# Kernel tuning notes

Measured on AMD Instinct MI355X. Metric: run time of the kernel, lower is better.

The kernel has to match this reference:

```python
import jax, jax.numpy as jnp
import numpy as np

D = 256; NH = 8; NL = 4; NP = 4; DFF = 1024; BS = 8; NQ = 300
DH = D // NH
EPS = 1e-5
SPATIAL = np.array([[100, 150], [50, 75], [25, 38], [13, 19]], dtype=np.int64)  # (H, W) per level
SIZES = (SPATIAL[:, 0] * SPATIAL[:, 1])
S = int(SIZES.sum())  # 19947
LSI = np.concatenate([[0], np.cumsum(SIZES)[:-1]]).astype(np.int64)


def setup_inputs() -> dict:
    key = jax.random.key(0)
    ks = iter(jax.random.split(key, 48))
    def nrm(shape, s=0.02):
        return jax.random.normal(next(ks), shape, jnp.float32) * s
    return {
        "tgt": jax.random.normal(next(ks), (BS, NQ, D), jnp.float32),
        "tgt_query_pos": jax.random.normal(next(ks), (BS, NQ, D), jnp.float32),
        "tgt_reference_points": jax.random.uniform(next(ks), (BS, NQ, NL, 2), jnp.float32),
        "memory": jax.random.normal(next(ks), (BS, S, D), jnp.float32),
        "memory_key_padding_mask": jnp.zeros((BS, S), jnp.bool_),
        "memory_spatial_shapes": jnp.asarray(SPATIAL),
        "memory_level_start_index": jnp.asarray(LSI),
        # self-attention (nn.MultiheadAttention) params
        "in_proj_w": nrm((3 * D, D)), "in_proj_b": jnp.zeros((3 * D,), jnp.float32),
        "out_proj_w": nrm((D, D)), "out_proj_b": jnp.zeros((D,), jnp.float32),
        # layernorms
        "norm1_g": jnp.ones((D,), jnp.float32), "norm1_b": jnp.zeros((D,), jnp.float32),
        "norm2_g": jnp.ones((D,), jnp.float32), "norm2_b": jnp.zeros((D,), jnp.float32),
        "norm3_g": jnp.ones((D,), jnp.float32), "norm3_b": jnp.zeros((D,), jnp.float32),
        # MSDeformAttn params
        "samp_off_w": nrm((NH * NL * NP * 2, D)), "samp_off_b": nrm((NH * NL * NP * 2,), 0.5),
        "attn_wt_w": nrm((NH * NL * NP, D)), "attn_wt_b": jnp.zeros((NH * NL * NP,), jnp.float32),
        "value_w": nrm((D, D)), "value_b": jnp.zeros((D,), jnp.float32),
        "outp_w": nrm((D, D)), "outp_b": jnp.zeros((D,), jnp.float32),
        # FFN params
        "lin1_w": nrm((DFF, D)), "lin1_b": jnp.zeros((DFF,), jnp.float32),
        "lin2_w": nrm((D, DFF)), "lin2_b": jnp.zeros((D,), jnp.float32),
    }


def _ln(x, g, b):
    m = x.mean(-1, keepdims=True)
    v = ((x - m) ** 2).mean(-1, keepdims=True)
    return (x - m) / jnp.sqrt(v + EPS) * g + b


def _self_attn(tgt, pos, in_w, in_b, ow, ob):
    bs, nq, _ = tgt.shape
    qk = tgt + pos
    qw, kw, vw = jnp.split(in_w, 3, axis=0)
    qb, kb, vb = jnp.split(in_b, 3)
    proj = lambda x, w, b: (x @ w.T + b).reshape(bs, nq, NH, DH)
    qh, kh, vh = proj(qk, qw, qb), proj(qk, kw, kb), proj(tgt, vw, vb)
    logits = jnp.einsum('bqhd,bkhd->bhqk', qh, kh) / np.sqrt(DH).astype(np.float32)
    a = jax.nn.softmax(logits, axis=-1)
    o = jnp.einsum('bhqk,bkhd->bqhd', a, vh).reshape(bs, nq, D)
    return o @ ow.T + ob


def _msdeform(query, ref, memory, pad_mask, so_w, so_b, aw_w, aw_b, vw, vb, ow, ob):
    bs, nq, _ = query.shape
    value = memory @ vw.T + vb
    value = jnp.where(pad_mask[..., None], 0.0, value).reshape(bs, S, NH, DH)
    off = (query @ so_w.T + so_b).reshape(bs, nq, NH, NL, NP, 2)
    aw = jax.nn.softmax((query @ aw_w.T + aw_b).reshape(bs, nq, NH, NL * NP), axis=-1)
    aw = aw.reshape(bs, nq, NH, NL, NP)
    # offset normalizer is (W, H) per level
    normalizer = jnp.asarray(SPATIAL[:, ::-1].copy(), jnp.float32)
    locs = ref[:, :, None, :, None, :] + off / normalizer[None, None, None, :, None, :]
    out = jnp.zeros((bs, nq, NH, DH), jnp.float32)
    for l in range(NL):
        Hl, Wl = int(SPATIAL[l, 0]), int(SPATIAL[l, 1])
        s0 = int(LSI[l])
        v = value[:, s0:s0 + Hl * Wl]  # [bs, Hl*Wl, NH, DH]
        # grid_sample(align_corners=False) pixel mapping
        x = locs[:, :, :, l, :, 0] * Wl - 0.5  # [bs, nq, NH, NP]
        y = locs[:, :, :, l, :, 1] * Hl - 0.5
        x0f, y0f = jnp.floor(x), jnp.floor(y)
        tx, ty = x - x0f, y - y0f
        x0, y0 = x0f.astype(jnp.int32), y0f.astype(jnp.int32)
        samp = jnp.zeros(x.shape + (DH,), jnp.float32)
        for dy, dx, w in ((0, 0, (1 - ty) * (1 - tx)), (0, 1, (1 - ty) * tx),
                          (1, 0, ty * (1 - tx)), (1, 1, ty * tx)):
            xi, yi = x0 + dx, y0 + dy
            valid = (xi >= 0) & (xi < Wl) & (yi >= 0) & (yi < Hl)  # zero padding
            idx = jnp.clip(yi, 0, Hl - 1) * Wl + jnp.clip(xi, 0, Wl - 1)
            idx2 = idx.swapaxes(2, 3).reshape(bs, nq * NP, NH)
            g = jnp.take_along_axis(v, idx2[..., None], axis=1)  # [bs, nq*NP, NH, DH]
            g = g.reshape(bs, nq, NP, NH, DH).transpose(0, 1, 3, 2, 4)
            samp = samp + g * (w * valid)[..., None]
        out = out + jnp.einsum('bqhp,bqhpd->bqhd', aw[:, :, :, l], samp)
    return out.reshape(bs, nq, D) @ ow.T + ob


def reference(tgt, tgt_query_pos, tgt_reference_points, memory, memory_key_padding_mask,
              memory_spatial_shapes, memory_level_start_index,
              in_proj_w, in_proj_b, out_proj_w, out_proj_b,
              norm1_g, norm1_b, norm2_g, norm2_b, norm3_g, norm3_b,
              samp_off_w, samp_off_b, attn_wt_w, attn_wt_b,
              value_w, value_b, outp_w, outp_b,
              lin1_w, lin1_b, lin2_w, lin2_b):
    # self-cross ordering (self_cross=True), eval mode (dropout=identity)
    t2 = _self_attn(tgt, tgt_query_pos, in_proj_w, in_proj_b, out_proj_w, out_proj_b)
    tgt = _ln(tgt + t2, norm2_g, norm2_b)
    t2 = _msdeform(tgt + tgt_query_pos, tgt_reference_points, memory, memory_key_padding_mask,
                   samp_off_w, samp_off_b, attn_wt_w, attn_wt_b, value_w, value_b, outp_w, outp_b)
    tgt = _ln(tgt + t2, norm1_g, norm1_b)
    t2 = jax.nn.relu(tgt @ lin1_w.T + lin1_b) @ lin2_w.T + lin2_b
    return _ln(tgt + t2, norm3_g, norm3_b)
```

## Files before the change

kernel.cpp:

```cpp
#include <hip/hip_runtime.h>
#include <hip/hip_bf16.h>

#define D_   256
#define NH_  8
#define NL_  4
#define NP_  4
#define DFF_ 1024
#define BS_  8
#define NQ_  300
#define DH_  32
#define S_TOT 19947
#define EPS_ 1e-5f

typedef __bf16 bf16x8 __attribute__((ext_vector_type(8)));
typedef __bf16 bf16x4 __attribute__((ext_vector_type(4)));
typedef float  f32x4  __attribute__((ext_vector_type(4)));

#define W_INW  0
#define W_OUTW 196608
#define W_SOW  262144
#define W_AWW  327680
#define W_VW   360448
#define W_OPW  425984
#define W_L1W  491520
#define W_L2W  753664
#define W_TOT  1015808

__global__ __launch_bounds__(256) void cast_w_kernel(
    const float* __restrict__ s_inw, const float* __restrict__ s_outw,
    const float* __restrict__ s_sow, const float* __restrict__ s_aww,
    const float* __restrict__ s_vw,  const float* __restrict__ s_opw,
    const float* __restrict__ s_l1w, const float* __restrict__ s_l2w,
    __bf16* __restrict__ dst)
{
    const int i = (blockIdx.x * 256 + threadIdx.x) * 4;
    if (i >= W_TOT) return;
    const float* s; int off;
    if      (i < W_OUTW) { s = s_inw;  off = W_INW;  }
    else if (i < W_SOW)  { s = s_outw; off = W_OUTW; }
    else if (i < W_AWW)  { s = s_sow;  off = W_SOW;  }
    else if (i < W_VW)   { s = s_aww;  off = W_AWW;  }
    else if (i < W_OPW)  { s = s_vw;   off = W_VW;   }
    else if (i < W_L1W)  { s = s_opw;  off = W_OPW;  }
    else if (i < W_L2W)  { s = s_l1w;  off = W_L1W;  }
    else                 { s = s_l2w;  off = W_L2W;  }
    const float4 v = *(const float4*)(s + (i - off));
    bf16x4 o;
    o[0] = (__bf16)v.x; o[1] = (__bf16)v.y;
    o[2] = (__bf16)v.z; o[3] = (__bf16)v.w;
    *(bf16x4*)(dst + i) = o;
}

__global__ __launch_bounds__(256) void rearrange_vw_kernel(
    const __bf16* __restrict__ W, __bf16* __restrict__ Wf)
{
    const int g = blockIdx.x * 256 + threadIdx.x;
    const int l = g & 63;
    const int t = (g >> 6) & 15;
    const int s = g >> 10;
    const int row = t * 16 + (l & 15);
    const int col = s * 32 + (l >> 4) * 8;
    *(bf16x8*)(Wf + (size_t)g * 8) = *(const bf16x8*)(W + (size_t)row * 256 + col);
}

__global__ __launch_bounds__(512, 4) void gemm_value(
    const float* __restrict__ A, const __bf16* __restrict__ Wf,
    const float* __restrict__ bias, __hip_bfloat16* __restrict__ C, int M)
{
    __shared__ __align__(16) __bf16 As[2][16][264];
    const int tid = threadIdx.x;
    const int wave = tid >> 6, lane = tid & 63;
    const int frow = lane & 15;
    const int k8 = (lane >> 4) * 8;

    bf16x8 bB[2][8];
#pragma unroll
    for (int j = 0; j < 2; ++j) {
        const int t = wave * 2 + j;
#pragma unroll
        for (int s = 0; s < 8; ++s)
            bB[j][s] = *(const bf16x8*)(Wf + ((size_t)(s * 16 + t) * 64 + lane) * 8);
    }
    float bb0 = bias[wave * 32 + frow];
    float bb1 = bias[wave * 32 + 16 + frow];

    const int nt = (M + 15) >> 4;
    const int stride = gridDim.x;
    int tile = blockIdx.x;

    const int srow = tid >> 5;
    const int scol = (tid & 31) * 8;

    {
        int gr = tile * 16 + srow; if (gr >= M) gr = M - 1;
        const float* ap = A + (size_t)gr * 256 + scol;
        const float4 a0 = *(const float4*)ap;
        const float4 a1 = *(const float4*)(ap + 4);
        bf16x8 o;
        o[0] = (__bf16)a0.x; o[1] = (__bf16)a0.y;
        o[2] = (__bf16)a0.z; o[3] = (__bf16)a0.w;
        o[4] = (__bf16)a1.x; o[5] = (__bf16)a1.y;
        o[6] = (__bf16)a1.z; o[7] = (__bf16)a1.w;
        *(bf16x8*)&As[0][srow][scol] = o;
    }
    __syncthreads();

    int buf = 0;
    for (; tile < nt; tile += stride, buf ^= 1) {
        const int nxt = tile + stride;
        const bool have_nxt = nxt < nt;
        float4 p0, p1;
        if (have_nxt) {
            int gr = nxt * 16 + srow; if (gr >= M) gr = M - 1;
            const float* ap = A + (size_t)gr * 256 + scol;
            p0 = *(const float4*)ap;
            p1 = *(const float4*)(ap + 4);
        }

        f32x4 acc0 = (f32x4){0.f, 0.f, 0.f, 0.f};
        f32x4 acc1 = acc0;
#pragma unroll
        for (int s = 0; s < 8; ++s) {
            const bf16x8 aF = *(const bf16x8*)&As[buf][frow][s * 32 + k8];
            acc0 = __builtin_amdgcn_mfma_f32_16x16x32_bf16(aF, bB[0][s], acc0, 0, 0, 0);
            acc1 = __builtin_amdgcn_mfma_f32_16x16x32_bf16(aF, bB[1][s], acc1, 0, 0, 0);
        }

        const int m0 = tile * 16;
        const int row0 = (lane >> 4) * 4;
        const int col0 = wave * 32 + frow;
#pragma unroll
        for (int r = 0; r < 4; ++r) {
            const int gr = m0 + row0 + r;
            if (gr < M) {
                __hip_bfloat16* cp = C + (size_t)gr * 256 + col0;
                cp[0]  = __float2bfloat16(acc0[r] + bb0);
                cp[16] = __float2bfloat16(acc1[r] + bb1);
            }
        }

        if (have_nxt) {
            bf16x8 o;
            o[0] = (__bf16)p0.x; o[1] = (__bf16)p0.y;
            o[2] = (__bf16)p0.z; o[3] = (__bf16)p0.w;
            o[4] = (__bf16)p1.x; o[5] = (__bf16)p1.y;
            o[6] = (__bf16)p1.z; o[7] = (__bf16)p1.w;
            *(bf16x8*)&As[buf ^ 1][srow][scol] = o;
        }
        __syncthreads();
    }
}

__global__ __launch_bounds__(256) void gemm_small(
    const float* __restrict__ A, const float* __restrict__ A2,
    const __bf16* __restrict__ W, const float* __restrict__ bias,
    float* __restrict__ C, int M, int N, int K, int relu)
{
    __shared__ __align__(16) __bf16 As[64][40];
    __shared__ __align__(16) __bf16 Bs[64][40];
    const int tid = threadIdx.x;
    const int wave = tid >> 6, lane = tid & 63;
    const int m0 = blockIdx.x * 64, n0 = blockIdx.y * 64;
    const int frow = lane & 15, fk = (lane >> 4) * 8;

    f32x4 acc[4];
#pragma unroll
    for (int j = 0; j < 4; ++j) acc[j] = (f32x4){0.f, 0.f, 0.f, 0.f};

    const int ar = tid >> 2;
    const int ak = (tid & 3) * 8;
    const bool a_ok = (m0 + ar) < M;

    for (int k0 = 0; k0 < K; k0 += 32) {
        float4 a0 = make_float4(0,0,0,0), a1 = a0;
        if (a_ok) {
            const float* ap = A + (size_t)(m0 + ar) * K + k0 + ak;
            a0 = *(const float4*)ap;
            a1 = *(const float4*)(ap + 4);
            if (A2) {
                const float* ap2 = A2 + (size_t)(m0 + ar) * K + k0 + ak;
                const float4 c0 = *(const float4*)ap2;
                const float4 c1 = *(const float4*)(ap2 + 4);
                a0.x += c0.x; a0.y += c0.y; a0.z += c0.z; a0.w += c0.w;
                a1.x += c1.x; a1.y += c1.y; a1.z += c1.z; a1.w += c1.w;
            }
        }
        const bf16x8 b8 = *(const bf16x8*)(W + (size_t)(n0 + ar) * K + k0 + ak);

        __syncthreads();
        bf16x8 w0;
        w0[0] = (__bf16)a0.x; w0[1] = (__bf16)a0.y; w0[2] = (__bf16)a0.z; w0[3] = (__bf16)a0.w;
        w0[4] = (__bf16)a1.x; w0[5] = (__bf16)a1.y; w0[6] = (__bf16)a1.z; w0[7] = (__bf16)a1.w;
        *(bf16x8*)&As[ar][ak] = w0;
        *(bf16x8*)&Bs[ar][ak] = b8;
        __syncthreads();

        const bf16x8 aF = *(const bf16x8*)&As[wave * 16 + frow][fk];
#pragma unroll
        for (int j = 0; j < 4; ++j) {
            const bf16x8 bF = *(const bf16x8*)&Bs[j * 16 + frow][fk];
            acc[j] = __builtin_amdgcn_mfma_f32_16x16x32_bf16(aF, bF, acc[j], 0, 0, 0);
        }
    }

    const int row = m0 + wave * 16 + (lane >> 4) * 4;
#pragma unroll
    for (int j = 0; j < 4; ++j) {
        const int col = n0 + j * 16 + frow;
        const float bb = bias[col];
#pragma unroll
        for (int r = 0; r < 4; ++r) {
            if (row + r >= M) continue;
            float val = acc[j][r] + bb;
            if (relu) val = fmaxf(val, 0.f);
            C[(size_t)(row + r) * N + col] = val;
        }
    }
}

__global__ __launch_bounds__(256) void attn_logits_kernel(
    const float* __restrict__ qk, __bf16* __restrict__ P)
{
    const int qt = blockIdx.x, bh = blockIdx.y;
    const int b = bh >> 3, h = bh & 7;
    const int wave = threadIdx.x >> 6, lane = threadIdx.x & 63;
    const int m = qt * 64 + wave * 16 + (lane & 15);
    const int k8 = (lane >> 4) * 8;
    const float scale = 0.17677669529663687f;

    bf16x8 aF = {};
    if (m < NQ_) {
        const float* qp = qk + (size_t)(b * NQ_ + m) * 512 + h * 32 + k8;
        const float4 q0 = *(const float4*)qp;
        const float4 q1 = *(const float4*)(qp + 4);
        aF[0] = (__bf16)q0.x; aF[1] = (__bf16)q0.y;
        aF[2] = (__bf16)q0.z; aF[3] = (__bf16)q0.w;
        aF[4] = (__bf16)q1.x; aF[5] = (__bf16)q1.y;
        aF[6] = (__bf16)q1.z; aF[7] = (__bf16)q1.w;
    }

    f32x4 c[19];
#pragma unroll
    for (int t = 0; t < 19; ++t) {
        const int n = t * 16 + (lane & 15);
        bf16x8 bF = {};
        if (n < NQ_) {
            const float* kp = qk + (size_t)(b * NQ_ + n) * 512 + 256 + h * 32 + k8;
            const float4 k0 = *(const float4*)kp;
            const float4 k1 = *(const float4*)(kp + 4);
            bF[0] = (__bf16)k0.x; bF[1] = (__bf16)k0.y;
            bF[2] = (__bf16)k0.z; bF[3] = (__bf16)k0.w;
            bF[4] = (__bf16)k1.x; bF[5] = (__bf16)k1.y;
            bF[6] = (__bf16)k1.z; bF[7] = (__bf16)k1.w;
        }
        f32x4 z = (f32x4){0.f, 0.f, 0.f, 0.f};
        c[t] = __builtin_amdgcn_mfma_f32_16x16x32_bf16(aF, bF, z, 0, 0, 0);
    }

    const int myc = lane & 15;
#pragma unroll
    for (int t = 0; t < 19; ++t) {
        const bool ok = (t * 16 + myc) < NQ_;
#pragma unroll
        for (int r = 0; r < 4; ++r)
            c[t][r] = ok ? c[t][r] * scale : -1e30f;
    }

    float mx[4] = {-1e30f, -1e30f, -1e30f, -1e30f};
#pragma unroll
    for (int t = 0; t < 19; ++t)
#pragma unroll
        for (int r = 0; r < 4; ++r) mx[r] = fmaxf(mx[r], c[t][r]);
#pragma unroll
    for (int off = 8; off; off >>= 1)
#pragma unroll
        for (int r = 0; r < 4; ++r)
            mx[r] = fmaxf(mx[r], __shfl_xor(mx[r], off, 64));

    float sum[4] = {0.f, 0.f, 0.f, 0.f};
#pragma unroll
    for (int t = 0; t < 19; ++t)
#pragma unroll
        for (int r = 0; r < 4; ++r) {
            const float e = __expf(c[t][r] - mx[r]);
            c[t][r] = e;
            sum[r] += e;
        }
#pragma unroll
    for (int off = 8; off; off >>= 1)
#pragma unroll
        for (int r = 0; r < 4; ++r)
            sum[r] += __shfl_xor(sum[r], off, 64);
    float inv[4];
#pragma unroll
    for (int r = 0; r < 4; ++r) inv[r] = 1.f / sum[r];

    __bf16* Pr = P + (size_t)bh * NQ_ * 320;
    const int row0 = qt * 64 + wave * 16 + (lane >> 4) * 4;
#pragma unroll
    for (int t = 0; t < 19; ++t) {
        const int col = t * 16 + myc;
        if (col >= NQ_) continue;
#pragma unroll
        for (int r = 0; r < 4; ++r)
            if (row0 + r < NQ_)
                Pr[(size_t)(row0 + r) * 320 + col] = (__bf16)(c[t][r] * inv[r]);
    }
}

__global__ __launch_bounds__(256) void attn_pv_kernel(
    const __bf16* __restrict__ P, const float* __restrict__ v,
    float* __restrict__ attn)
{
    __shared__ __align__(16) __bf16 Vt[32][328];
    const int qt = blockIdx.x, bh = blockIdx.y;
    const int b = bh >> 3, h = bh & 7;
    const int tid = threadIdx.x;

    {
        const int d = tid & 31;
        for (int kk = tid >> 5; kk < NQ_; kk += 8)
            Vt[d][kk] = (__bf16)v[(size_t)(b * NQ_ + kk) * 256 + h * 32 + d];
        for (int i = tid; i < 32 * 20; i += 256)
            Vt[i & 31][300 + (i >> 5)] = (__bf16)0.f;
    }
    __syncthreads();

    const int wave = tid >> 6, lane = tid & 63;
    const int mrow = qt * 64 + wave * 16 + (lane & 15);
    const int k8 = (lane >> 4) * 8;
    const __bf16* Pr = P + (size_t)bh * NQ_ * 320;

    f32x4 acc0 = (f32x4){0.f, 0.f, 0.f, 0.f};
    f32x4 acc1 = acc0;
#pragma unroll
    for (int k0 = 0; k0 < 320; k0 += 32) {
        bf16x8 aF = {};
        if (mrow < NQ_) aF = *(const bf16x8*)(Pr + (size_t)mrow * 320 + k0 + k8);
        const bf16x8 b0 = *(const bf16x8*)&Vt[lane & 15][k0 + k8];
        const bf16x8 b1 = *(const bf16x8*)&Vt[16 + (lane & 15)][k0 + k8];
        acc0 = __builtin_amdgcn_mfma_f32_16x16x32_bf16(aF, b0, acc0, 0, 0, 0);
        acc1 = __builtin_amdgcn_mfma_f32_16x16x32_bf16(aF, b1, acc1, 0, 0, 0);
    }

    const int row0 = qt * 64 + wave * 16 + (lane >> 4) * 4;
    const int col = lane & 15;
#pragma unroll
    for (int r = 0; r < 4; ++r) {
        if (row0 + r >= NQ_) continue;
        float* op = attn + (size_t)(b * NQ_ + row0 + r) * 256 + h * 32;
        op[col]      = acc0[r];
        op[col + 16] = acc1[r];
    }
}

__global__ __launch_bounds__(256) void ln_kernel(
    const float* __restrict__ x, const float* __restrict__ res,
    const float* __restrict__ g, const float* __restrict__ bt,
    float* __restrict__ out,
    const float* __restrict__ pos, float* __restrict__ out2)
{
    const int row = blockIdx.x;
    const int tid = threadIdx.x;
    const size_t idx = (size_t)row * D_ + tid;
    float v = x[idx] + (res ? res[idx] : 0.f);

    __shared__ float red[4];
    float s = v;
#pragma unroll
    for (int off = 32; off; off >>= 1) s += __shfl_xor(s, off, 64);
    if ((tid & 63) == 0) red[tid >> 6] = s;
    __syncthreads();
    const float mean = (red[0] + red[1] + red[2] + red[3]) * (1.f / D_);
    const float c = v - mean;
    __syncthreads();

    float s2 = c * c;
#pragma unroll
    for (int off = 32; off; off >>= 1) s2 += __shfl_xor(s2, off, 64);
    if ((tid & 63) == 0) red[tid >> 6] = s2;
    __syncthreads();
    const float var = (red[0] + red[1] + red[2] + red[3]) * (1.f / D_);

    const float y = c * rsqrtf(var + EPS_) * g[tid] + bt[tid];
    out[idx] = y;
    if (out2) out2[idx] = y + pos[idx];
}

__global__ __launch_bounds__(256) void msdeform_kernel(
    const float* __restrict__ offs, const float* __restrict__ awl,
    const float* __restrict__ refp, const __hip_bfloat16* __restrict__ value,
    float* __restrict__ samp)
{
    const int row = blockIdx.x;
    const int b = row / NQ_;
    const int tid = threadIdx.x;
    const int h = tid >> 5, d = tid & 31;

    __shared__ float off_s[256];
    __shared__ float aw_s[128];
    __shared__ float ref_s[8];
    off_s[tid] = offs[(size_t)row * 256 + tid];
    if (tid < 128) aw_s[tid] = awl[(size_t)row * 128 + tid];
    if (tid < 8) ref_s[tid] = refp[(size_t)row * 8 + tid];
    __syncthreads();

    float mx = -1e30f;
#pragma unroll
    for (int i = 0; i < 16; ++i) mx = fmaxf(mx, aw_s[h * 16 + i]);
    float sum = 0.f;
#pragma unroll
    for (int i = 0; i < 16; ++i) sum += __expf(aw_s[h * 16 + i] - mx);
    const float winv = 1.f / sum;

    const int Hs[4] = {100, 50, 25, 13};
    const int Wl_[4] = {150, 75, 38, 19};
    const int S0[4] = {0, 15000, 18750, 19700};

    float o = 0.f;
    const __hip_bfloat16* vbase = value + ((size_t)b * S_TOT) * D_ + h * 32 + d;

#pragma unroll
    for (int l = 0; l < NL_; ++l) {
        const int Hl = Hs[l], Wl = Wl_[l];
        const float rx = ref_s[l * 2], ry = ref_s[l * 2 + 1];
        const __hip_bfloat16* vl = vbase + (size_t)S0[l] * D_;
#pragma unroll
        for (int p = 0; p < NP_; ++p) {
            const int oi = ((h * NL_ + l) * NP_ + p) * 2;
            const float lx = rx + off_s[oi] / (float)Wl;
            const float ly = ry + off_s[oi + 1] / (float)Hl;
            const float x = lx * Wl - 0.5f;
            const float y = ly * Hl - 0.5f;
            const float x0f = floorf(x), y0f = floorf(y);
            const float tx = x - x0f, ty = y - y0f;
            const int x0 = (int)x0f, y0 = (int)y0f;
            const float aw = __expf(aw_s[h * 16 + l * 4 + p] - mx) * winv;

            float sacc = 0.f;
#pragma unroll
            for (int cc = 0; cc < 4; ++cc) {
                const int dy = cc >> 1, dx = cc & 1;
                const int xi = x0 + dx, yi = y0 + dy;
                const float w = (dy ? ty : 1.f - ty) * (dx ? tx : 1.f - tx);
                if (xi >= 0 && xi < Wl && yi >= 0 && yi < Hl) {
                    const int idx = yi * Wl + xi;
                    sacc += w * __bfloat162float(vl[(size_t)idx * D_]);
                }
            }
            o += aw * sacc;
        }
    }
    samp[(size_t)row * 256 + tid] = o;
}

extern "C" void kernel_launch(void* const* d_in, const int* in_sizes, int n_in,
                              void* d_out, int out_size, void* d_ws, size_t ws_size,
                              hipStream_t stream)
{
    const float* tgt   = (const float*)d_in[0];
    const float* pos   = (const float*)d_in[1];
    const float* refp  = (const float*)d_in[2];
    const float* memory= (const float*)d_in[3];
    const float* in_w  = (const float*)d_in[7];
    const float* in_b  = (const float*)d_in[8];
    const float* outw  = (const float*)d_in[9];
    const float* outb  = (const float*)d_in[10];
    const float* n1g = (const float*)d_in[11]; const float* n1b = (const float*)d_in[12];
    const float* n2g = (const float*)d_in[13]; const float* n2b = (const float*)d_in[14];
    const float* n3g = (const float*)d_in[15]; const float* n3b = (const float*)d_in[16];
    const float* sow = (const float*)d_in[17]; const float* sob = (const float*)d_in[18];
    const float* aww = (const float*)d_in[19]; const float* awb = (const float*)d_in[20];
    const float* vw  = (const float*)d_in[21]; const float* vb_ = (const float*)d_in[22];
    const float* opw = (const float*)d_in[23]; const float* opb = (const float*)d_in[24];
    const float* l1w = (const float*)d_in[25]; const float* l1b = (const float*)d_in[26];
    const float* l2w = (const float*)d_in[27]; const float* l2b = (const float*)d_in[28];
    float* out = (float*)d_out;

    char* ws = (char*)d_ws;
    size_t o = 0;
    auto alloc = [&](size_t bytes) -> char* {
        char* p = ws + o;
        o += (bytes + 255) & ~(size_t)255;
        return p;
    };

    const int M = BS_ * NQ_;
    __bf16* Wb = (__bf16*)alloc((size_t)W_TOT * 2);
    __bf16* Wf = (__bf16*)alloc((size_t)65536 * 2);
    __hip_bfloat16* value = (__hip_bfloat16*)alloc((size_t)BS_ * S_TOT * D_ * 2);
    __bf16* P    = (__bf16*)alloc((size_t)64 * NQ_ * 320 * 2);
    float* qk    = (float*)alloc((size_t)M * 512 * 4);
    float* v     = (float*)alloc((size_t)M * 256 * 4);
    float* attn  = (float*)alloc((size_t)M * 256 * 4);
    float* attno = (float*)alloc((size_t)M * 256 * 4);
    float* tgt1  = (float*)alloc((size_t)M * 256 * 4);
    float* query2= (float*)alloc((size_t)M * 256 * 4);
    float* offs  = (float*)alloc((size_t)M * 256 * 4);
    float* awl   = (float*)alloc((size_t)M * 128 * 4);
    float* samp  = (float*)alloc((size_t)M * 256 * 4);
    float* t2m   = (float*)alloc((size_t)M * 256 * 4);
    float* tgt2  = (float*)alloc((size_t)M * 256 * 4);
    float* ffn1  = (float*)alloc((size_t)M * 1024 * 4);
    float* ffn2  = (float*)alloc((size_t)M * 256 * 4);

    const dim3 blk(256);
    const int MB = (M + 63) / 64;

    cast_w_kernel<<<(W_TOT / 4 + 255) / 256, blk, 0, stream>>>(
        in_w, outw, sow, aww, vw, opw, l1w, l2w, Wb);
    rearrange_vw_kernel<<<32, blk, 0, stream>>>(Wb + W_VW, Wf);

    gemm_small<<<dim3(MB, 8), blk, 0, stream>>>(tgt, pos, Wb + W_INW, in_b, qk, M, 512, 256, 0);
    gemm_small<<<dim3(MB, 4), blk, 0, stream>>>(tgt, nullptr, Wb + W_INW + 512 * 256, in_b + 512, v, M, 256, 256, 0);
    attn_logits_kernel<<<dim3(5, 64), blk, 0, stream>>>(qk, P);
    attn_pv_kernel<<<dim3(5, 64), blk, 0, stream>>>(P, v, attn);
    gemm_small<<<dim3(MB, 4), blk, 0, stream>>>(attn, nullptr, Wb + W_OUTW, outb, attno, M, 256, 256, 0);
    ln_kernel<<<M, blk, 0, stream>>>(tgt, attno, n2g, n2b, tgt1, pos, query2);

    gemm_small<<<dim3(MB, 4), blk, 0, stream>>>(query2, nullptr, Wb + W_SOW, sob, offs, M, 256, 256, 0);
    gemm_small<<<dim3(MB, 2), blk, 0, stream>>>(query2, nullptr, Wb + W_AWW, awb, awl, M, 128, 256, 0);
    gemm_value<<<dim3(512), dim3(512), 0, stream>>>(memory, Wf, vb_, value, BS_ * S_TOT);
    msdeform_kernel<<<M, blk, 0, stream>>>(offs, awl, refp, value, samp);
    gemm_small<<<dim3(MB, 4), blk, 0, stream>>>(samp, nullptr, Wb + W_OPW, opb, t2m, M, 256, 256, 0);
    ln_kernel<<<M, blk, 0, stream>>>(tgt1, t2m, n1g, n1b, tgt2, nullptr, nullptr);

    gemm_small<<<dim3(MB, 16), blk, 0, stream>>>(tgt2, nullptr, Wb + W_L1W, l1b, ffn1, M, 1024, 256, 1);
    gemm_small<<<dim3(MB, 4), blk, 0, stream>>>(ffn1, nullptr, Wb + W_L2W, l2b, ffn2, M, 256, 1024, 0);
    ln_kernel<<<M, blk, 0, stream>>>(tgt2, ffn2, n3g, n3b, out, nullptr, nullptr);
}
```

Measured before the change: 476.8 us.

## Fuse self-attention logits and PV, merge offset/weight GEMMs, vectorize deform sampling

The softmax-logits and P·V kernels are merged into one kernel that keeps the probability tile in shared memory instead of writing it to global memory. The sampling-offset and attention-weight projections become a single GEMM launch that writes to two outputs. The deformable-sampling kernel now handles two queries per block, and each thread reads two bf16 channels with one 32-bit load. Together these cut launches, global round-trips and per-channel gather loads, at the cost of more shared memory per block in the fused attention kernel.

```diff
diff --git a/kernel.cpp b/kernel.cpp
--- a/kernel.cpp
+++ b/kernel.cpp
@@ -154,7 +154,8 @@
 __global__ __launch_bounds__(256) void gemm_small(
     const float* __restrict__ A, const float* __restrict__ A2,
     const __bf16* __restrict__ W, const float* __restrict__ bias,
-    float* __restrict__ C, int M, int N, int K, int relu)
+    float* __restrict__ C, int M, int N, int K, int relu,
+    const float* __restrict__ bias2, float* __restrict__ C2, int N1)
 {
     __shared__ __align__(16) __bf16 As[64][40];
     __shared__ __align__(16) __bf16 Bs[64][40];
@@ -207,26 +208,44 @@
 #pragma unroll
     for (int j = 0; j < 4; ++j) {
         const int col = n0 + j * 16 + frow;
-        const float bb = bias[col];
+        float* dst; const float* bsrc; int strideC, ccol;
+        if (!C2 || col < N1) { dst = C;  bsrc = bias;  strideC = N1;     ccol = col; }
+        else                 { dst = C2; bsrc = bias2; strideC = N - N1; ccol = col - N1; }
+        const float bb = bsrc[ccol];
 #pragma unroll
         for (int r = 0; r < 4; ++r) {
             if (row + r >= M) continue;
             float val = acc[j][r] + bb;
             if (relu) val = fmaxf(val, 0.f);
-            C[(size_t)(row + r) * N + col] = val;
-        }
-    }
-}
-
-__global__ __launch_bounds__(256) void attn_logits_kernel(
-    const float* __restrict__ qk, __bf16* __restrict__ P)
-{
+            dst[(size_t)(row + r) * strideC + ccol] = val;
+        }
+    }
+}
+
+__global__ __launch_bounds__(256) void attn_fused_kernel(
+    const float* __restrict__ qk, const float* __restrict__ v,
+    float* __restrict__ attn)
+{
+    __shared__ __align__(16) __bf16 Vt[32][328];
+    __shared__ __align__(16) __bf16 Ps[64][328];
     const int qt = blockIdx.x, bh = blockIdx.y;
     const int b = bh >> 3, h = bh & 7;
-    const int wave = threadIdx.x >> 6, lane = threadIdx.x & 63;
+    const int tid = threadIdx.x;
+    const int wave = tid >> 6, lane = tid & 63;
+    const float scale = 0.17677669529663687f;
+
+    {
+        const int d = tid & 31;
+        for (int kk = tid >> 5; kk < NQ_; kk += 8)
+            Vt[d][kk] = (__bf16)v[(size_t)(b * NQ_ + kk) * 256 + h * 32 + d];
+        for (int i = tid; i < 32 * 20; i += 256)
+            Vt[i & 31][300 + (i >> 5)] = (__bf16)0.f;
+        for (int i = tid; i < 64 * 16; i += 256)
+            Ps[i & 63][304 + (i >> 6)] = (__bf16)0.f;
+    }
+
     const int m = qt * 64 + wave * 16 + (lane & 15);
     const int k8 = (lane >> 4) * 8;
-    const float scale = 0.17677669529663687f;
 
     bf16x8 aF = {};
     if (m < NQ_) {
@@ -295,55 +314,29 @@
 #pragma unroll
     for (int r = 0; r < 4; ++r) inv[r] = 1.f / sum[r];
 
-    __bf16* Pr = P + (size_t)bh * NQ_ * 320;
-    const int row0 = qt * 64 + wave * 16 + (lane >> 4) * 4;
+    const int lrow0 = wave * 16 + (lane >> 4) * 4;
 #pragma unroll
     for (int t = 0; t < 19; ++t) {
         const int col = t * 16 + myc;
-        if (col >= NQ_) continue;
 #pragma unroll
         for (int r = 0; r < 4; ++r)
-            if (row0 + r < NQ_)
-                Pr[(size_t)(row0 + r) * 320 + col] = (__bf16)(c[t][r] * inv[r]);
-    }
-}
-
-__global__ __launch_bounds__(256) void attn_pv_kernel(
-    const __bf16* __restrict__ P, const float* __restrict__ v,
-    float* __restrict__ attn)
-{
-    __shared__ __align__(16) __bf16 Vt[32][328];
-    const int qt = blockIdx.x, bh = blockIdx.y;
-    const int b = bh >> 3, h = bh & 7;
-    const int tid = threadIdx.x;
-
-    {
-        const int d = tid & 31;
-        for (int kk = tid >> 5; kk < NQ_; kk += 8)
-            Vt[d][kk] = (__bf16)v[(size_t)(b * NQ_ + kk) * 256 + h * 32 + d];
-        for (int i = tid; i < 32 * 20; i += 256)
-            Vt[i & 31][300 + (i >> 5)] = (__bf16)0.f;
+            Ps[lrow0 + r][col] = (__bf16)(c[t][r] * inv[r]);
     }
     __syncthreads();
 
-    const int wave = tid >> 6, lane = tid & 63;
-    const int mrow = qt * 64 + wave * 16 + (lane & 15);
-    const int k8 = (lane >> 4) * 8;
-    const __bf16* Pr = P + (size_t)bh * NQ_ * 320;
-
+    const int lm = wave * 16 + (lane & 15);
     f32x4 acc0 = (f32x4){0.f, 0.f, 0.f, 0.f};
     f32x4 acc1 = acc0;
 #pragma unroll
     for (int k0 = 0; k0 < 320; k0 += 32) {
-        bf16x8 aF = {};
-        if (mrow < NQ_) aF = *(const bf16x8*)(Pr + (size_t)mrow * 320 + k0 + k8);
+        const bf16x8 pF = *(const bf16x8*)&Ps[lm][k0 + k8];
         const bf16x8 b0 = *(const bf16x8*)&Vt[lane & 15][k0 + k8];
         const bf16x8 b1 = *(const bf16x8*)&Vt[16 + (lane & 15)][k0 + k8];
-        acc0 = __builtin_amdgcn_mfma_f32_16x16x32_bf16(aF, b0, acc0, 0, 0, 0);
-        acc1 = __builtin_amdgcn_mfma_f32_16x16x32_bf16(aF, b1, acc1, 0, 0, 0);
-    }
-
-    const int row0 = qt * 64 + wave * 16 + (lane >> 4) * 4;
+        acc0 = __builtin_amdgcn_mfma_f32_16x16x32_bf16(pF, b0, acc0, 0, 0, 0);
+        acc1 = __builtin_amdgcn_mfma_f32_16x16x32_bf16(pF, b1, acc1, 0, 0, 0);
+    }
+
+    const int row0 = qt * 64 + lrow0;
     const int col = lane & 15;
 #pragma unroll
     for (int r = 0; r < 4; ++r) {
@@ -392,52 +385,54 @@
     const float* __restrict__ refp, const __hip_bfloat16* __restrict__ value,
     float* __restrict__ samp)
 {
-    const int row = blockIdx.x;
+    const int half = threadIdx.x >> 7;
+    const int row = blockIdx.x * 2 + half;
     const int b = row / NQ_;
-    const int tid = threadIdx.x;
-    const int h = tid >> 5, d = tid & 31;
-
-    __shared__ float off_s[256];
-    __shared__ float aw_s[128];
-    __shared__ float ref_s[8];
-    off_s[tid] = offs[(size_t)row * 256 + tid];
-    if (tid < 128) aw_s[tid] = awl[(size_t)row * 128 + tid];
-    if (tid < 8) ref_s[tid] = refp[(size_t)row * 8 + tid];
+    const int t = threadIdx.x & 127;
+    const int h = t >> 4, d2 = t & 15;
+
+    __shared__ float off_s[2][256];
+    __shared__ float aw_s[2][128];
+    __shared__ float ref_s[2][8];
+    off_s[half][t]       = offs[(size_t)row * 256 + t];
+    off_s[half][t + 128] = offs[(size_t)row * 256 + t + 128];
+    aw_s[half][t]        = awl[(size_t)row * 128 + t];
+    if (t < 8) ref_s[half][t] = refp[(size_t)row * 8 + t];
     __syncthreads();
 
     float mx = -1e30f;
 #pragma unroll
-    for (int i = 0; i < 16; ++i) mx = fmaxf(mx, aw_s[h * 16 + i]);
+    for (int i = 0; i < 16; ++i) mx = fmaxf(mx, aw_s[half][h * 16 + i]);
     float sum = 0.f;
 #pragma unroll
-    for (int i = 0; i < 16; ++i) sum += __expf(aw_s[h * 16 + i] - mx);
+    for (int i = 0; i < 16; ++i) sum += __expf(aw_s[half][h * 16 + i] - mx);
     const float winv = 1.f / sum;
 
     const int Hs[4] = {100, 50, 25, 13};
     const int Wl_[4] = {150, 75, 38, 19};
     const int S0[4] = {0, 15000, 18750, 19700};
 
-    float o = 0.f;
-    const __hip_bfloat16* vbase = value + ((size_t)b * S_TOT) * D_ + h * 32 + d;
+    float o0 = 0.f, o1 = 0.f;
+    const __hip_bfloat16* vbase = value + ((size_t)b * S_TOT) * D_ + h * 32 + d2 * 2;
 
 #pragma unroll
     for (int l = 0; l < NL_; ++l) {
         const int Hl = Hs[l], Wl = Wl_[l];
-        const float rx = ref_s[l * 2], ry = ref_s[l * 2 + 1];
+        const float rx = ref_s[half][l * 2], ry = ref_s[half][l * 2 + 1];
         const __hip_bfloat16* vl = vbase + (size_t)S0[l] * D_;
 #pragma unroll
         for (int p = 0; p < NP_; ++p) {
             const int oi = ((h * NL_ + l) * NP_ + p) * 2;
-            const float lx = rx + off_s[oi] / (float)Wl;
-            const float ly = ry + off_s[oi + 1] / (float)Hl;
+            const float lx = rx + off_s[half][oi] / (float)Wl;
+            const float ly = ry + off_s[half][oi + 1] / (float)Hl;
             const float x = lx * Wl - 0.5f;
             const float y = ly * Hl - 0.5f;
             const float x0f = floorf(x), y0f = floorf(y);
             const float tx = x - x0f, ty = y - y0f;
             const int x0 = (int)x0f, y0 = (int)y0f;
-            const float aw = __expf(aw_s[h * 16 + l * 4 + p] - mx) * winv;
-
-            float sacc = 0.f;
+            const float aw = __expf(aw_s[half][h * 16 + l * 4 + p] - mx) * winv;
+
+            float s0 = 0.f, s1 = 0.f;
 #pragma unroll
             for (int cc = 0; cc < 4; ++cc) {
                 const int dy = cc >> 1, dx = cc & 1;
@@ -445,13 +440,17 @@
                 const float w = (dy ? ty : 1.f - ty) * (dx ? tx : 1.f - tx);
                 if (xi >= 0 && xi < Wl && yi >= 0 && yi < Hl) {
                     const int idx = yi * Wl + xi;
-                    sacc += w * __bfloat162float(vl[(size_t)idx * D_]);
+                    const unsigned u = *(const unsigned*)(vl + (size_t)idx * D_);
+                    s0 += w * __uint_as_float(u << 16);
+                    s1 += w * __uint_as_float(u & 0xffff0000u);
                 }
             }
-            o += aw * sacc;
-        }
-    }
-    samp[(size_t)row * 256 + tid] = o;
+            o0 += aw * s0;
+            o1 += aw * s1;
+        }
+    }
+    float2 ov; ov.x = o0; ov.y = o1;
+    *(float2*)(samp + (size_t)row * 256 + h * 32 + d2 * 2) = ov;
 }
 
 extern "C" void kernel_launch(void* const* d_in, const int* in_sizes, int n_in,
@@ -489,7 +488,6 @@
     __bf16* Wb = (__bf16*)alloc((size_t)W_TOT * 2);
     __bf16* Wf = (__bf16*)alloc((size_t)65536 * 2);
     __hip_bfloat16* value = (__hip_bfloat16*)alloc((size_t)BS_ * S_TOT * D_ * 2);
-    __bf16* P    = (__bf16*)alloc((size_t)64 * NQ_ * 320 * 2);
     float* qk    = (float*)alloc((size_t)M * 512 * 4);
     float* v     = (float*)alloc((size_t)M * 256 * 4);
     float* attn  = (float*)alloc((size_t)M * 256 * 4);
@@ -511,21 +509,19 @@
         in_w, outw, sow, aww, vw, opw, l1w, l2w, Wb);
     rearrange_vw_kernel<<<32, blk, 0, stream>>>(Wb + W_VW, Wf);
 
-    gemm_small<<<dim3(MB, 8), blk, 0, stream>>>(tgt, pos, Wb + W_INW, in_b, qk, M, 512, 256, 0);
-    gemm_small<<<dim3(MB, 4), blk, 0, stream>>>(tgt, nullptr, Wb + W_INW + 512 * 256, in_b + 512, v, M, 256, 256, 0);
-    attn_logits_kernel<<<dim3(5, 64), blk, 0, stream>>>(qk, P);
-    attn_pv_kernel<<<dim3(5, 64), blk, 0, stream>>>(P, v, attn);
-    gemm_small<<<dim3(MB, 4), blk, 0, stream>>>(attn, nullptr, Wb + W_OUTW, outb, attno, M, 256, 256, 0);
+    gemm_small<<<dim3(MB, 8), blk, 0, stream>>>(tgt, pos, Wb + W_INW, in_b, qk, M, 512, 256, 0, nullptr, nullptr, 512);
+    gemm_small<<<dim3(MB, 4), blk, 0, stream>>>(tgt, nullptr, Wb + W_INW + 512 * 256, in_b + 512, v, M, 256, 256, 0, nullptr, nullptr, 256);
+    attn_fused_kernel<<<dim3(5, 64), blk, 0, stream>>>(qk, v, attn);
+    gemm_small<<<dim3(MB, 4), blk, 0, stream>>>(attn, nullptr, Wb + W_OUTW, outb, attno, M, 256, 256, 0, nullptr, nullptr, 256);
     ln_kernel<<<M, blk, 0, stream>>>(tgt, attno, n2g, n2b, tgt1, pos, query2);
 
-    gemm_small<<<dim3(MB, 4), blk, 0, stream>>>(query2, nullptr, Wb + W_SOW, sob, offs, M, 256, 256, 0);
-    gemm_small<<<dim3(MB, 2), blk, 0, stream>>>(query2, nullptr, Wb + W_AWW, awb, awl, M, 128, 256, 0);
+    gemm_small<<<dim3(MB, 6), blk, 0, stream>>>(query2, nullptr, Wb + W_SOW, sob, offs, M, 384, 256, 0, awb, awl, 256);
     gemm_value<<<dim3(512), dim3(512), 0, stream>>>(memory, Wf, vb_, value, BS_ * S_TOT);
-    msdeform_kernel<<<M, blk, 0, stream>>>(offs, awl, refp, value, samp);
-    gemm_small<<<dim3(MB, 4), blk, 0, stream>>>(samp, nullptr, Wb + W_OPW, opb, t2m, M, 256, 256, 0);
+    msdeform_kernel<<<M / 2, blk, 0, stream>>>(offs, awl, refp, value, samp);
+    gemm_small<<<dim3(MB, 4), blk, 0, stream>>>(samp, nullptr, Wb + W_OPW, opb, t2m, M, 256, 256, 0, nullptr, nullptr, 256);
     ln_kernel<<<M, blk, 0, stream>>>(tgt1, t2m, n1g, n1b, tgt2, nullptr, nullptr);
 
-    gemm_small<<<dim3(MB, 16), blk, 0, stream>>>(tgt2, nullptr, Wb + W_L1W, l1b, ffn1, M, 1024, 256, 1);
-    gemm_small<<<dim3(MB, 4), blk, 0, stream>>>(ffn1, nullptr, Wb + W_L2W, l2b, ffn2, M, 256, 1024, 0);
+    gemm_small<<<dim3(MB, 16), blk, 0, stream>>>(tgt2, nullptr, Wb + W_L1W, l1b, ffn1, M, 1024, 256, 1, nullptr, nullptr, 1024);
+    gemm_small<<<dim3(MB, 4), blk, 0, stream>>>(ffn1, nullptr, Wb + W_L2W, l2b, ffn2, M, 256, 1024, 0, nullptr, nullptr, 256);
     ln_kernel<<<M, blk, 0, stream>>>(tgt2, ffn2, n3g, n3b, out, nullptr, nullptr);
 }
```

Result: faster. 447.6 us (-6.1%).
